# Kernel optimization log

Measured on AMD Instinct MI355X. Metric: run time of the kernel, lower is better.

The kernel has to match this reference:

```python
import jax, jax.numpy as jnp
import numpy as np

EPS = 1e-06
HIDDEN = 8

def setup_inputs() -> dict:
    key = jax.random.key(0)
    k1, k2, k3, k4, k5 = jax.random.split(key, 5)
    B = 8388608
    p = jax.random.uniform(k1, (B, 3), dtype=jnp.float32)
    # Linear params, PyTorch default init: U(-1/sqrt(fan_in), 1/sqrt(fan_in))
    b1_lim = 1.0 / np.sqrt(3.0)
    b2_lim = 1.0 / np.sqrt(HIDDEN)
    W1 = jax.random.uniform(k2, (HIDDEN, 3), jnp.float32, -b1_lim, b1_lim)
    b1 = jax.random.uniform(k3, (HIDDEN,), jnp.float32, -b1_lim, b1_lim)
    W2 = jax.random.uniform(k4, (3, HIDDEN), jnp.float32, -b2_lim, b2_lim)
    b2 = jax.random.uniform(k5, (3,), jnp.float32, -b2_lim, b2_lim)
    return {"p": p, "W1": W1, "b1": b1, "W2": W2, "b2": b2}

def reference(p, W1, b1, W2, b2):
    p = jnp.clip(p, EPS, 1.0 - EPS)
    z = jnp.log(p) - jnp.log1p(-p)            # logit, [B,3]
    h = jnp.tanh(z @ W1.T + b1)               # [B,8]
    s = h @ W2.T + b2                         # [B,3]
    a = jax.nn.softmax(s, axis=-1)            # [B,3]
    fused_logit = jnp.sum(a * z, axis=-1, keepdims=True)  # [B,1]
    fused_prob = jax.nn.sigmoid(fused_logit)
    return (fused_prob, a)
```

## Files before the change

kernel.cpp:

```cpp
#include <hip/hip_runtime.h>
#include <math.h>

#define EPS 1e-6f
#define INVLN2 1.4426950408889634f
#define TWOINVLN2 2.8853900817779268f

typedef float f32x4 __attribute__((ext_vector_type(4)));
typedef float f32x2 __attribute__((ext_vector_type(2)));

__device__ __forceinline__ float log2_hw(float x) { return __builtin_amdgcn_logf(x); }
__device__ __forceinline__ float exp2_hw(float x) { return __builtin_amdgcn_exp2f(x); }
__device__ __forceinline__ float rcp_hw(float x)  { return __builtin_amdgcn_rcpf(x); }

__device__ __forceinline__ f32x2 bc2(float s)      { f32x2 v = {s, s}; return v; }
__device__ __forceinline__ f32x2 fma2(f32x2 a, f32x2 b, f32x2 c) {
    return __builtin_elementwise_fma(a, b, c);
}
__device__ __forceinline__ f32x2 exp2_v2(f32x2 x) {
    f32x2 r = {exp2_hw(x.x), exp2_hw(x.y)}; return r;
}
__device__ __forceinline__ f32x2 log2_v2(f32x2 x) {
    f32x2 r = {log2_hw(x.x), log2_hw(x.y)}; return r;
}
__device__ __forceinline__ f32x2 rcp_v2(f32x2 x) {
    f32x2 r = {rcp_hw(x.x), rcp_hw(x.y)}; return r;
}

__device__ __forceinline__ void point_eval2(
    f32x2 q0, f32x2 q1, f32x2 q2,
    const float w1d[8][3], const float b1s[8],
    const float w2n[3][8], const float cc[3],
    f32x2& prob, f32x2& a0, f32x2& a1, f32x2& a2)
{
    const f32x2 lo = bc2(EPS), hi = bc2(1.0f - EPS), one = bc2(1.0f);
    f32x2 pc0 = __builtin_elementwise_min(__builtin_elementwise_max(q0, lo), hi);
    f32x2 pc1 = __builtin_elementwise_min(__builtin_elementwise_max(q1, lo), hi);
    f32x2 pc2 = __builtin_elementwise_min(__builtin_elementwise_max(q2, lo), hi);
    f32x2 zl0 = log2_v2(pc0) - log2_v2(one - pc0);
    f32x2 zl1 = log2_v2(pc1) - log2_v2(one - pc1);
    f32x2 zl2 = log2_v2(pc2) - log2_v2(one - pc2);

    f32x2 s0 = bc2(cc[0]), s1 = bc2(cc[1]), s2 = bc2(cc[2]);
    #pragma unroll
    for (int j = 0; j < 8; ++j) {
        f32x2 arg = fma2(bc2(w1d[j][0]), zl0,
                    fma2(bc2(w1d[j][1]), zl1,
                    fma2(bc2(w1d[j][2]), zl2, bc2(b1s[j]))));
        f32x2 r = rcp_v2(exp2_v2(arg) + one);
        s0 = fma2(bc2(w2n[0][j]), r, s0);
        s1 = fma2(bc2(w2n[1][j]), r, s1);
        s2 = fma2(bc2(w2n[2][j]), r, s2);
    }

    f32x2 e0 = exp2_v2(s0);
    f32x2 e1 = exp2_v2(s1);
    f32x2 e2 = exp2_v2(s2);
    f32x2 rden = rcp_v2(e0 + e1 + e2);
    a0 = e0 * rden; a1 = e1 * rden; a2 = e2 * rden;

    f32x2 fl2 = fma2(a0, zl0, fma2(a1, zl1, a2 * zl2));
    prob = rcp_v2(one + exp2_v2(-fl2));
}

__global__ __launch_bounds__(256) void attn_fusion_kernel(
    const float* __restrict__ p,
    const float* __restrict__ W1,
    const float* __restrict__ b1,
    const float* __restrict__ W2,
    const float* __restrict__ b2,
    float* __restrict__ out_prob,
    float* __restrict__ out_a,
    int ngroups)
{
    int t = blockIdx.x * blockDim.x + threadIdx.x;
    if (t >= ngroups) return;

    float w1d[8][3], b1s[8], w2n[3][8], cc[3];
    #pragma unroll
    for (int j = 0; j < 8; ++j) {
        #pragma unroll
        for (int k = 0; k < 3; ++k) w1d[j][k] = 2.0f * W1[j * 3 + k];
        b1s[j] = b1[j] * TWOINVLN2;
    }
    #pragma unroll
    for (int k = 0; k < 3; ++k) {
        float sum = 0.0f;
        #pragma unroll
        for (int j = 0; j < 8; ++j) {
            float w2s = W2[k * 8 + j] * INVLN2;
            w2n[k][j] = -2.0f * w2s;
            sum += w2s;
        }
        cc[k] = b2[k] * INVLN2 + sum;
    }

    const f32x4* pv = reinterpret_cast<const f32x4*>(p) + (size_t)t * 3;
    f32x4 v0 = pv[0];
    f32x4 v1 = pv[1];
    f32x4 v2 = pv[2];
    float in[12] = {v0.x, v0.y, v0.z, v0.w,
                    v1.x, v1.y, v1.z, v1.w,
                    v2.x, v2.y, v2.z, v2.w};

    f32x2 qA0 = {in[0], in[3]}, qA1 = {in[1], in[4]}, qA2 = {in[2], in[5]};
    f32x2 qB0 = {in[6], in[9]}, qB1 = {in[7], in[10]}, qB2 = {in[8], in[11]};

    f32x2 prA, aA0, aA1, aA2;
    f32x2 prB, aB0, aB1, aB2;
    point_eval2(qA0, qA1, qA2, w1d, b1s, w2n, cc, prA, aA0, aA1, aA2);
    point_eval2(qB0, qB1, qB2, w1d, b1s, w2n, cc, prB, aB0, aB1, aB2);

    f32x4 pr = {prA.x, prA.y, prB.x, prB.y};
    reinterpret_cast<f32x4*>(out_prob)[t] = pr;

    f32x4* ao = reinterpret_cast<f32x4*>(out_a) + (size_t)t * 3;
    f32x4 o0 = {aA0.x, aA1.x, aA2.x, aA0.y};
    f32x4 o1 = {aA1.y, aA2.y, aB0.x, aB1.x};
    f32x4 o2 = {aB2.x, aB0.y, aB1.y, aB2.y};
    ao[0] = o0;
    ao[1] = o1;
    ao[2] = o2;
}

__global__ void attn_fusion_tail(
    const float* __restrict__ p,
    const float* __restrict__ W1,
    const float* __restrict__ b1,
    const float* __restrict__ W2,
    const float* __restrict__ b2,
    float* __restrict__ out_prob,
    float* __restrict__ out_a,
    int start, int B)
{
    int i = start + blockIdx.x * blockDim.x + threadIdx.x;
    if (i >= B) return;

    float zl[3];
    #pragma unroll
    for (int k = 0; k < 3; ++k) {
        float pc = fminf(fmaxf(p[(size_t)i * 3 + k], EPS), 1.0f - EPS);
        zl[k] = log2_hw(pc) - log2_hw(1.0f - pc);
    }

    float s[3];
    #pragma unroll
    for (int k = 0; k < 3; ++k) {
        float sum = 0.0f;
        #pragma unroll
        for (int j = 0; j < 8; ++j) sum += W2[k * 8 + j] * INVLN2;
        s[k] = b2[k] * INVLN2 + sum;
    }
    #pragma unroll
    for (int j = 0; j < 8; ++j) {
        float arg = b1[j] * TWOINVLN2;
        #pragma unroll
        for (int k = 0; k < 3; ++k) arg = fmaf(2.0f * W1[j * 3 + k], zl[k], arg);
        float r = rcp_hw(exp2_hw(arg) + 1.0f);
        #pragma unroll
        for (int k = 0; k < 3; ++k) s[k] = fmaf(-2.0f * W2[k * 8 + j] * INVLN2, r, s[k]);
    }
    float e0 = exp2_hw(s[0]), e1 = exp2_hw(s[1]), e2 = exp2_hw(s[2]);
    float rden = rcp_hw(e0 + e1 + e2);
    float a0 = e0 * rden, a1 = e1 * rden, a2 = e2 * rden;
    out_a[(size_t)i * 3 + 0] = a0;
    out_a[(size_t)i * 3 + 1] = a1;
    out_a[(size_t)i * 3 + 2] = a2;
    float fl2 = fmaf(a0, zl[0], fmaf(a1, zl[1], a2 * zl[2]));
    out_prob[i] = rcp_hw(1.0f + exp2_hw(-fl2));
}

extern "C" void kernel_launch(void* const* d_in, const int* in_sizes, int n_in,
                              void* d_out, int out_size, void* d_ws, size_t ws_size,
                              hipStream_t stream) {
    const float* p  = (const float*)d_in[0];
    const float* W1 = (const float*)d_in[1];
    const float* b1 = (const float*)d_in[2];
    const float* W2 = (const float*)d_in[3];
    const float* b2 = (const float*)d_in[4];

    int B = in_sizes[0] / 3;
    float* out_prob = (float*)d_out;
    float* out_a    = (float*)d_out + B;

    int ngroups = B / 4;
    if (ngroups > 0) {
        int block = 256;
        int grid = (ngroups + block - 1) / block;
        attn_fusion_kernel<<<grid, block, 0, stream>>>(
            p, W1, b1, W2, b2, out_prob, out_a, ngroups);
    }
    int tail = B - ngroups * 4;
    if (tail > 0) {
        attn_fusion_tail<<<1, 64, 0, stream>>>(
            p, W1, b1, W2, b2, out_prob, out_a, ngroups * 4, B);
    }
}
```

Baseline: 41.95 us.

## Use grid-stride persistent loop with software-prefetched next input group

Replaces the one-thread-per-group launch with a fixed 2048-block grid in which each thread walks groups in a grid-stride loop. The loads for the next group are issued before computing the current one, so memory latency can overlap with compute. Weight setup is also amortised over many groups per thread. The cost is extra registers for the prefetched vectors and fewer resident waves overall, which may reduce how well the GPU hides latency on its own.

```diff
diff --git a/kernel.cpp b/kernel.cpp
--- a/kernel.cpp
+++ b/kernel.cpp
@@ -72,8 +72,8 @@
     float* __restrict__ out_a,
     int ngroups)
 {
-    int t = blockIdx.x * blockDim.x + threadIdx.x;
-    if (t >= ngroups) return;
+    int tid = blockIdx.x * blockDim.x + threadIdx.x;
+    int nthreads = gridDim.x * blockDim.x;
 
     float w1d[8][3], b1s[8], w2n[3][8], cc[3];
     #pragma unroll
@@ -94,32 +94,50 @@
         cc[k] = b2[k] * INVLN2 + sum;
     }
 
-    const f32x4* pv = reinterpret_cast<const f32x4*>(p) + (size_t)t * 3;
-    f32x4 v0 = pv[0];
-    f32x4 v1 = pv[1];
-    f32x4 v2 = pv[2];
-    float in[12] = {v0.x, v0.y, v0.z, v0.w,
-                    v1.x, v1.y, v1.z, v1.w,
-                    v2.x, v2.y, v2.z, v2.w};
-
-    f32x2 qA0 = {in[0], in[3]}, qA1 = {in[1], in[4]}, qA2 = {in[2], in[5]};
-    f32x2 qB0 = {in[6], in[9]}, qB1 = {in[7], in[10]}, qB2 = {in[8], in[11]};
-
-    f32x2 prA, aA0, aA1, aA2;
-    f32x2 prB, aB0, aB1, aB2;
-    point_eval2(qA0, qA1, qA2, w1d, b1s, w2n, cc, prA, aA0, aA1, aA2);
-    point_eval2(qB0, qB1, qB2, w1d, b1s, w2n, cc, prB, aB0, aB1, aB2);
-
-    f32x4 pr = {prA.x, prA.y, prB.x, prB.y};
-    reinterpret_cast<f32x4*>(out_prob)[t] = pr;
-
-    f32x4* ao = reinterpret_cast<f32x4*>(out_a) + (size_t)t * 3;
-    f32x4 o0 = {aA0.x, aA1.x, aA2.x, aA0.y};
-    f32x4 o1 = {aA1.y, aA2.y, aB0.x, aB1.x};
-    f32x4 o2 = {aB2.x, aB0.y, aB1.y, aB2.y};
-    ao[0] = o0;
-    ao[1] = o1;
-    ao[2] = o2;
+    const f32x4* p4 = reinterpret_cast<const f32x4*>(p);
+    f32x4* pr4 = reinterpret_cast<f32x4*>(out_prob);
+    f32x4* a4  = reinterpret_cast<f32x4*>(out_a);
+
+    int t = tid;
+    if (t >= ngroups) return;
+
+    f32x4 v0 = p4[(size_t)t * 3 + 0];
+    f32x4 v1 = p4[(size_t)t * 3 + 1];
+    f32x4 v2 = p4[(size_t)t * 3 + 2];
+
+    while (true) {
+        int tn = t + nthreads;
+        bool more = tn < ngroups;
+
+        f32x4 n0, n1, n2;
+        if (more) {
+            n0 = p4[(size_t)tn * 3 + 0];
+            n1 = p4[(size_t)tn * 3 + 1];
+            n2 = p4[(size_t)tn * 3 + 2];
+        }
+
+        f32x2 qA0 = {v0.x, v0.w}, qA1 = {v0.y, v1.x}, qA2 = {v0.z, v1.y};
+        f32x2 qB0 = {v1.z, v2.y}, qB1 = {v1.w, v2.z}, qB2 = {v2.x, v2.w};
+
+        f32x2 prA, aA0, aA1, aA2;
+        f32x2 prB, aB0, aB1, aB2;
+        point_eval2(qA0, qA1, qA2, w1d, b1s, w2n, cc, prA, aA0, aA1, aA2);
+        point_eval2(qB0, qB1, qB2, w1d, b1s, w2n, cc, prB, aB0, aB1, aB2);
+
+        f32x4 pr = {prA.x, prA.y, prB.x, prB.y};
+        pr4[t] = pr;
+
+        f32x4 o0 = {aA0.x, aA1.x, aA2.x, aA0.y};
+        f32x4 o1 = {aA1.y, aA2.y, aB0.x, aB1.x};
+        f32x4 o2 = {aB2.x, aB0.y, aB1.y, aB2.y};
+        a4[(size_t)t * 3 + 0] = o0;
+        a4[(size_t)t * 3 + 1] = o1;
+        a4[(size_t)t * 3 + 2] = o2;
+
+        if (!more) break;
+        v0 = n0; v1 = n1; v2 = n2;
+        t = tn;
+    }
 }
 
 __global__ void attn_fusion_tail(
@@ -185,7 +203,9 @@
     int ngroups = B / 4;
     if (ngroups > 0) {
         int block = 256;
-        int grid = (ngroups + block - 1) / block;
+        int grid = 2048;
+        int max_grid = (ngroups + block - 1) / block;
+        if (grid > max_grid) grid = max_grid;
         attn_fusion_kernel<<<grid, block, 0, stream>>>(
             p, W1, b1, W2, b2, out_prob, out_a, ngroups);
     }
```

New measurement: 43.99 us. +4.9%, slower.
